# Performance work log

Measured on AMD Instinct MI355X. Metric: run time of the kernel, lower is better.

The kernel has to match this reference:

```python
import jax, jax.numpy as jnp
import numpy as np

EPS = 1e-5

def _subsys_level(x, W, b, g, beta):
    # x: [S,B,I], W: [S,O,I]  -> Linear -> Tanh -> BatchNorm(batch stats over B)
    h = jnp.einsum('sbi,soi->sbo', x, W) + b[:, None, :]
    h = jnp.tanh(h)
    mu = jnp.mean(h, axis=1, keepdims=True)
    var = jnp.var(h, axis=1, keepdims=True)
    return g[:, None, :] * (h - mu) * jax.lax.rsqrt(var + EPS) + beta[:, None, :]

def setup_inputs() -> dict:
    key = jax.random.key(0)
    ks = jax.random.split(key, 16)
    B, N = 4096, 6000
    u = lambda k, shp: jax.random.uniform(k, shp, jnp.float32, -0.001, 0.001)
    return {
        'mutant_state': jax.random.uniform(ks[0], (B, N), jnp.float32),
        'gene_idx': jax.random.randint(ks[1], (512, 16), 0, N),
        'W1': u(ks[2], (512, 20, 16)), 'b1': u(ks[3], (512, 20)),
        'g1': jnp.ones((512, 20), jnp.float32), 'beta1': jnp.zeros((512, 20), jnp.float32),
        'W2': u(ks[4], (64, 24, 160)), 'b2': u(ks[5], (64, 24)),
        'g2': jnp.ones((64, 24), jnp.float32), 'beta2': jnp.zeros((64, 24), jnp.float32),
        'W3': u(ks[6], (8, 32, 192)), 'b3': u(ks[7], (8, 32)),
        'g3': jnp.ones((8, 32), jnp.float32), 'beta3': jnp.zeros((8, 32), jnp.float32),
        'Wr': u(ks[8], (64, 256)), 'br': u(ks[9], (64,)),
        'gr': jnp.ones((64,), jnp.float32), 'betar': jnp.zeros((64,), jnp.float32),
    }

def reference(mutant_state, gene_idx, W1, b1, g1, beta1, W2, b2, g2, beta2,
              W3, b3, g3, beta3, Wr, br, gr, betar):
    B = mutant_state.shape[0]
    # Level 1 (leaves): gather per-term gene mutant states -> [S1,B,G]
    x1 = jnp.transpose(mutant_state[:, gene_idx], (1, 0, 2))  # [512,B,16]
    o1 = _subsys_level(x1, W1, b1, g1, beta1)                  # [512,B,20]
    # Level 2: each of 64 parents concatenates 8 children outputs -> [64,B,160]
    x2 = o1.reshape(64, 8, B, 20).transpose(0, 2, 1, 3).reshape(64, B, 160)
    o2 = _subsys_level(x2, W2, b2, g2, beta2)                  # [64,B,24]
    # Level 3: 8 parents x 8 children -> [8,B,192]
    x3 = o2.reshape(8, 8, B, 24).transpose(0, 2, 1, 3).reshape(8, B, 192)
    o3 = _subsys_level(x3, W3, b3, g3, beta3)                  # [8,B,32]
    # Root: concat 8 outputs -> [B,256]
    xr = o3.transpose(1, 0, 2).reshape(B, 256)
    hr = jnp.tanh(xr @ Wr.T + br)
    mu = jnp.mean(hr, axis=0, keepdims=True)
    var = jnp.var(hr, axis=0, keepdims=True)
    return gr * (hr - mu) * jax.lax.rsqrt(var + EPS) + betar  # [B,64]
```

## Files before the change

kernel.cpp:

```cpp
#include <hip/hip_runtime.h>
#include <hip/hip_fp16.h>

#define BATCH 4096
#define EPS 1e-5f

typedef __half h16;
typedef float f32x2 __attribute__((ext_vector_type(2)));

union H8 { float4 f4; h16 h[8]; };
union H4 { float2 f2; h16 h[4]; __half2 h2[2]; };
union H2U { float f; __half2 h2; unsigned int u; };

__device__ __forceinline__ float tanh_fast(float x){
  float e = __expf(2.0f*x);
  return 1.0f - 2.0f*__builtin_amdgcn_rcpf(e + 1.0f);
}

__device__ __forceinline__ float wred(float v){
  #pragma unroll
  for (int off=32; off; off>>=1) v += __shfl_xor(v, off);
  return v;
}

__global__ __launch_bounds__(256) void k_transpose(const float* __restrict__ ms, h16* __restrict__ msT){
  __shared__ float tile[64][65];
  int tc = blockIdx.x * 64;
  int tb = blockIdx.y * 64;
  int tx = threadIdx.x & 63;
  int ty = threadIdx.x >> 6;
  #pragma unroll
  for (int k=0;k<16;++k){
    int r = ty + k*4;
    int c = tc + tx;
    if (c < 6000) tile[r][tx] = ms[(size_t)(tb + r)*6000 + c];
  }
  __syncthreads();
  #pragma unroll
  for (int k=0;k<16;++k){
    int r = ty + k*4;
    int c = tc + r;
    if (c < 6000) msT[(size_t)c*BATCH + tb + tx] = __float2half(tile[tx][r]);
  }
}

__global__ __launch_bounds__(64) void k_statsA(const h16* __restrict__ msT, const int* __restrict__ gidx,
    const float* __restrict__ W1, const float* __restrict__ b1,
    h16* __restrict__ H1, float* __restrict__ part1){
  const int s = blockIdx.y;
  const int bc = blockIdx.x;
  const int lane = threadIdx.x;
  const int b0 = bc*256 + lane*4;
  const float* Wp = W1 + s*320;
  f32x2 acc[20][2];
  #pragma unroll
  for (int o=0;o<20;++o){
    float bv = b1[s*20+o];
    acc[o][0] = (f32x2){bv,bv};
    acc[o][1] = (f32x2){bv,bv};
  }
  #pragma unroll 4
  for (int g=0; g<16; ++g){
    const int row = gidx[s*16+g]*BATCH;
    H4 u; u.f2 = *reinterpret_cast<const float2*>(msT + row + b0);
    float2 fa = __half22float2(u.h2[0]);
    float2 fb = __half22float2(u.h2[1]);
    f32x2 xa = (f32x2){fa.x, fa.y};
    f32x2 xb = (f32x2){fb.x, fb.y};
    #pragma unroll
    for (int o=0;o<20;++o){
      float wv = Wp[o*16+g];
      f32x2 w2 = (f32x2){wv,wv};
      acc[o][0] = __builtin_elementwise_fma(xa, w2, acc[o][0]);
      acc[o][1] = __builtin_elementwise_fma(xb, w2, acc[o][1]);
    }
  }
  #pragma unroll
  for (int o=0;o<20;++o){
    float h0=tanh_fast(acc[o][0].x), h1=tanh_fast(acc[o][0].y);
    float h2=tanh_fast(acc[o][1].x), h3=tanh_fast(acc[o][1].y);
    H4 u;
    u.h2[0] = __float22half2_rn(make_float2(h0,h1));
    u.h2[1] = __float22half2_rn(make_float2(h2,h3));
    *reinterpret_cast<float2*>(H1 + (size_t)(s*20+o)*BATCH + b0) = u.f2;
    float S = wred((h0+h1)+(h2+h3));
    float Q = wred((h0*h0+h1*h1)+(h2*h2+h3*h3));
    if (lane==0){
      part1[((s*20+o)*2  )*16 + bc] = S;
      part1[((s*20+o)*2+1)*16 + bc] = Q;
    }
  }
}

__global__ __launch_bounds__(256) void k_fold2(const float* __restrict__ W, const float* __restrict__ bb,
    const float* __restrict__ g, const float* __restrict__ beta,
    const float* __restrict__ part, float* __restrict__ Wf, float* __restrict__ bf){
  const int p = blockIdx.x;
  const int tid = threadIdx.x;
  __shared__ float aL[160], cL[160];
  for (int t = tid; t < 160; t += 256){
    int ch = p*160 + t;
    float S=0.f, Q=0.f;
    for (int bc=0; bc<16; ++bc){ S += part[(ch*2)*16 + bc]; Q += part[(ch*2+1)*16 + bc]; }
    float mu  = S * (1.0f/BATCH);
    float var = Q * (1.0f/BATCH) - mu*mu;
    float a = g[ch] * rsqrtf(var + EPS);
    aL[t] = a;
    cL[t] = beta[ch] - a*mu;
  }
  __syncthreads();
  const int NW = 160*24;
  for (int e = tid; e < NW; e += 256){
    int j = e % 24, i = e / 24;
    Wf[p*NW + e] = W[p*NW + j*160 + i] * aL[i];
  }
  if (tid < 24){
    float sv = bb[p*24 + tid];
    for (int i=0;i<160;++i) sv = fmaf(W[p*NW + tid*160 + i], cL[i], sv);
    bf[p*24 + tid] = sv;
  }
}

__global__ __launch_bounds__(256) void k_passB(const h16* __restrict__ H1,
    const float* __restrict__ W2f, const float* __restrict__ b2f,
    h16* __restrict__ H2, float* __restrict__ part2){
  const int p = blockIdx.y;
  const int bc = blockIdx.x;
  const int tid = threadIdx.x;
  const int wv = tid >> 6;
  const int lane = tid & 63;
  const int b = bc*256 + wv*64 + lane;
  const int bcw = bc*4 + wv;
  f32x2 acc2[12];
  #pragma unroll
  for (int j2=0;j2<12;++j2) acc2[j2] = (f32x2){b2f[p*24+2*j2], b2f[p*24+2*j2+1]};
  const h16* __restrict__ h1p = H1 + (size_t)p*160*BATCH + b;
  const float* __restrict__ w2p = W2f + p*3840;
  #pragma unroll 4
  for (int i=0;i<160;++i){
    float x = __half2float(h1p[(size_t)i*BATCH]);
    f32x2 x2 = (f32x2){x,x};
    #pragma unroll
    for (int j2=0;j2<12;++j2){
      f32x2 w2 = (f32x2){w2p[i*24+2*j2], w2p[i*24+2*j2+1]};
      acc2[j2] = __builtin_elementwise_fma(x2, w2, acc2[j2]);
    }
  }
  float v[24];
  #pragma unroll
  for (int j2=0;j2<12;++j2){
    v[2*j2]   = tanh_fast(acc2[j2].x);
    v[2*j2+1] = tanh_fast(acc2[j2].y);
  }
  {
    h16* dst = H2 + ((size_t)p*BATCH + b)*24;
    H8 u;
    #pragma unroll
    for (int t=0;t<3;++t){
      #pragma unroll
      for (int j=0;j<8;++j) u.h[j] = __float2half(v[t*8+j]);
      *reinterpret_cast<float4*>(dst + t*8) = u.f4;
    }
  }
  #pragma unroll
  for (int j=0;j<24;++j){
    float S = wred(v[j]);
    float Q = wred(v[j]*v[j]);
    if (lane==0){
      part2[((p*24+j)*2  )*64 + bcw] = S;
      part2[((p*24+j)*2+1)*64 + bcw] = Q;
    }
  }
}

__global__ __launch_bounds__(512) void k_passC(const h16* __restrict__ H2, const float* __restrict__ part2,
    const float* __restrict__ g2, const float* __restrict__ beta2,
    const float* __restrict__ W3, const float* __restrict__ b3,
    h16* __restrict__ H3, float* __restrict__ part3){
  const int q = blockIdx.y;
  const int bc = blockIdx.x;
  const int tid = threadIdx.x;
  const int wv = tid >> 6;
  const int lane = tid & 63;
  __shared__ float aL[192], cL[192];
  for (int t = tid; t < 192; t += 512){
    int ch = q*192 + t;
    float S=0.f, Q=0.f;
    for (int c=0;c<64;++c){ S += part2[(ch*2)*64 + c]; Q += part2[(ch*2+1)*64 + c]; }
    float mu  = S * (1.0f/BATCH);
    float var = Q * (1.0f/BATCH) - mu*mu;
    float a = g2[ch] * rsqrtf(var + EPS);
    aL[t] = a; cL[t] = beta2[ch] - a*mu;
  }
  __syncthreads();
  const int b = bc*64 + lane;
  const int jb = wv*4;
  float acc[4];
  #pragma unroll
  for (int j=0;j<4;++j) acc[j] = b3[q*32 + jb + j];
  for (int c2=0;c2<8;++c2){
    const h16* src = H2 + ((size_t)(q*8+c2)*BATCH + b)*24;
    float xn[24];
    #pragma unroll
    for (int t=0;t<3;++t){
      H8 u; u.f4 = *reinterpret_cast<const float4*>(src + t*8);
      #pragma unroll
      for (int i=0;i<8;++i){
        int ci = c2*24 + t*8 + i;
        xn[t*8+i] = fmaf(aL[ci], __half2float(u.h[i]), cL[ci]);
      }
    }
    #pragma unroll
    for (int j=0;j<4;++j){
      const float* wr = W3 + q*6144 + (jb+j)*192 + c2*24;
      #pragma unroll
      for (int i=0;i<24;++i) acc[j] = fmaf(xn[i], wr[i], acc[j]);
    }
  }
  #pragma unroll
  for (int j=0;j<4;++j) acc[j] = tanh_fast(acc[j]);
  {
    h16* dst = H3 + (size_t)b*256 + q*32 + jb;
    H2U u0,u1;
    u0.h2 = __halves2half2(__float2half(acc[0]), __float2half(acc[1]));
    u1.h2 = __halves2half2(__float2half(acc[2]), __float2half(acc[3]));
    float2 vv; vv.x = u0.f; vv.y = u1.f;
    *reinterpret_cast<float2*>(dst) = vv;
  }
  #pragma unroll
  for (int j=0;j<4;++j){
    float S = wred(acc[j]);
    float Q = wred(acc[j]*acc[j]);
    if (lane==0){
      part3[((q*32+jb+j)*2  )*64 + bc] = S;
      part3[((q*32+jb+j)*2+1)*64 + bc] = Q;
    }
  }
}

__global__ __launch_bounds__(256) void k_passD(const h16* __restrict__ H3, const float* __restrict__ part3,
    const float* __restrict__ g3, const float* __restrict__ beta3,
    const float* __restrict__ Wr, const float* __restrict__ br,
    float* __restrict__ Hr, float* __restrict__ partR){
  const int bc = blockIdx.x;
  const int jb = blockIdx.y * 8;
  const int tid = threadIdx.x;
  const int wv = tid >> 6;
  const int lane = tid & 63;
  __shared__ float aL[256], cL[256];
  __shared__ float lacc[4][64][9];
  {
    float S=0.f, Q=0.f;
    for (int c=0;c<64;++c){ S += part3[(tid*2)*64 + c]; Q += part3[(tid*2+1)*64 + c]; }
    float mu  = S * (1.0f/BATCH);
    float var = Q * (1.0f/BATCH) - mu*mu;
    float a = g3[tid] * rsqrtf(var + EPS);
    aL[tid] = a; cL[tid] = beta3[tid] - a*mu;
  }
  __syncthreads();
  const int b = bc*64 + lane;
  float acc[8];
  #pragma unroll
  for (int j=0;j<8;++j) acc[j] = 0.f;
  const h16* src = H3 + (size_t)b*256 + wv*64;
  #pragma unroll
  for (int kk=0; kk<8; ++kk){
    const int sl = wv*8 + kk;
    H8 u; u.f4 = *reinterpret_cast<const float4*>(src + kk*8);
    float xn[8];
    #pragma unroll
    for (int i=0;i<8;++i){
      int ci = sl*8+i;
      xn[i] = fmaf(aL[ci], __half2float(u.h[i]), cL[ci]);
    }
    #pragma unroll
    for (int j=0;j<8;++j){
      const float* wr = Wr + (jb+j)*256 + sl*8;
      #pragma unroll
      for (int i=0;i<8;++i) acc[j] = fmaf(xn[i], wr[i], acc[j]);
    }
  }
  #pragma unroll
  for (int j=0;j<8;++j) lacc[wv][lane][j] = acc[j];
  __syncthreads();
  #pragma unroll
  for (int k=0;k<2;++k){
    const int j = k*4 + wv;
    float v = br[jb+j] + (lacc[0][lane][j] + lacc[1][lane][j]) + (lacc[2][lane][j] + lacc[3][lane][j]);
    v = tanh_fast(v);
    Hr[(size_t)b*64 + jb + j] = v;
    float S = wred(v);
    float Q = wred(v*v);
    if (lane==0){
      partR[((jb+j)*2  )*64 + bc] = S;
      partR[((jb+j)*2+1)*64 + bc] = Q;
    }
  }
}

__global__ __launch_bounds__(256) void k_final(const float* __restrict__ Hr, const float* __restrict__ partR,
    const float* __restrict__ gr, const float* __restrict__ betar, float* __restrict__ out){
  __shared__ float aL[64], cL[64];
  const int tid = threadIdx.x;
  if (tid < 64){
    float S=0.f, Q=0.f;
    for (int bc=0; bc<64; ++bc){ S += partR[(tid*2)*64 + bc]; Q += partR[(tid*2+1)*64 + bc]; }
    float mu  = S * (1.0f/BATCH);
    float var = Q * (1.0f/BATCH) - mu*mu;
    float a = gr[tid] * rsqrtf(var + EPS);
    aL[tid] = a; cL[tid] = betar[tid] - a*mu;
  }
  __syncthreads();
  const int i4 = blockIdx.x*256 + tid;
  float4 v = *reinterpret_cast<const float4*>(Hr + (size_t)i4*4);
  int o = (i4*4)&63;
  float4 r;
  r.x = aL[o  ]*v.x + cL[o  ];
  r.y = aL[o+1]*v.y + cL[o+1];
  r.z = aL[o+2]*v.z + cL[o+2];
  r.w = aL[o+3]*v.w + cL[o+3];
  *reinterpret_cast<float4*>(out + (size_t)i4*4) = r;
}

extern "C" void kernel_launch(void* const* d_in, const int* in_sizes, int n_in,
                              void* d_out, int out_size, void* d_ws, size_t ws_size,
                              hipStream_t stream) {
  const float* ms    = (const float*)d_in[0];
  const int*   gidx  = (const int*)  d_in[1];
  const float* W1    = (const float*)d_in[2];
  const float* b1    = (const float*)d_in[3];
  const float* g1    = (const float*)d_in[4];
  const float* beta1 = (const float*)d_in[5];
  const float* W2    = (const float*)d_in[6];
  const float* b2    = (const float*)d_in[7];
  const float* g2    = (const float*)d_in[8];
  const float* beta2 = (const float*)d_in[9];
  const float* W3    = (const float*)d_in[10];
  const float* b3    = (const float*)d_in[11];
  const float* g3    = (const float*)d_in[12];
  const float* beta3 = (const float*)d_in[13];
  const float* Wr    = (const float*)d_in[14];
  const float* br    = (const float*)d_in[15];
  const float* gr    = (const float*)d_in[16];
  const float* betar = (const float*)d_in[17];
  float* out = (float*)d_out;

  char* w = (char*)d_ws;
  size_t off = 0;
  auto take = [&](size_t bytes)->char*{
    char* p = w + off;
    off = (off + bytes + 255) & ~(size_t)255;
    return p;
  };
  h16*   msT    = (h16*)  take((size_t)6000*BATCH*2);
  h16*   H1     = (h16*)  take((size_t)10240*BATCH*2);
  h16*   H2     = (h16*)  take((size_t)64*BATCH*24*2);
  h16*   H3     = (h16*)  take((size_t)BATCH*256*2);
  float* Hr     = (float*)take((size_t)BATCH*64*4);
  float* part1  = (float*)take((size_t)10240*2*16*4);
  float* part2  = (float*)take((size_t)1536*2*64*4);
  float* part3  = (float*)take((size_t)256*2*64*4);
  float* partR  = (float*)take((size_t)64*2*64*4);
  float* W2f    = (float*)take((size_t)64*24*160*4);
  float* b2f    = (float*)take((size_t)64*24*4);
  if (off > ws_size) return;

  k_transpose<<<dim3(94,64), 256, 0, stream>>>(ms, msT);
  k_statsA<<<dim3(16,512), 64, 0, stream>>>(msT, gidx, W1, b1, H1, part1);
  k_fold2<<<64, 256, 0, stream>>>(W2, b2, g1, beta1, part1, W2f, b2f);
  k_passB<<<dim3(16,64), 256, 0, stream>>>(H1, W2f, b2f, H2, part2);
  k_passC<<<dim3(64,8), 512, 0, stream>>>(H2, part2, g2, beta2, W3, b3, H3, part3);
  k_passD<<<dim3(64,8), 256, 0, stream>>>(H3, part3, g3, beta3, Wr, br, Hr, partR);
  k_final<<<256, 256, 0, stream>>>(Hr, partR, gr, betar, out);
}
```

Measured before the change: 185.4 us.

## Store level-1 activations interleaved per batch pair and widen statsA blocks

k_statsA now processes two batch elements per thread with 256-thread blocks and writes its outputs in a layout where each batch pair's 20 channels sit contiguously as packed half2 words. Channel-major stride-BATCH rows are replaced with per-subsystem, per-batch-pair records. k_passB reads this new layout, and the partial-stat buffers double to 32 wave slots, with k_fold2 updated to sum them. The aim is higher occupancy in statsA and more contiguous stores, at the cost of strided 2-byte reads in passB that stride 40 halves per batch pair.

```diff
diff --git a/kernel.cpp b/kernel.cpp
--- a/kernel.cpp
+++ b/kernel.cpp
@@ -8,7 +8,6 @@
 typedef float f32x2 __attribute__((ext_vector_type(2)));
 
 union H8 { float4 f4; h16 h[8]; };
-union H4 { float2 f2; h16 h[4]; __half2 h2[2]; };
 union H2U { float f; __half2 h2; unsigned int u; };
 
 __device__ __forceinline__ float tanh_fast(float x){
@@ -43,50 +42,48 @@
   }
 }
 
-__global__ __launch_bounds__(64) void k_statsA(const h16* __restrict__ msT, const int* __restrict__ gidx,
+__global__ __launch_bounds__(256) void k_statsA(const h16* __restrict__ msT, const int* __restrict__ gidx,
     const float* __restrict__ W1, const float* __restrict__ b1,
-    h16* __restrict__ H1, float* __restrict__ part1){
+    float* __restrict__ H1f, float* __restrict__ part1){
   const int s = blockIdx.y;
   const int bc = blockIdx.x;
-  const int lane = threadIdx.x;
-  const int b0 = bc*256 + lane*4;
+  const int tid = threadIdx.x;
+  const int wv = tid >> 6;
+  const int lane = tid & 63;
+  const int bp = bc*256 + tid;
+  const int b0 = bp*2;
   const float* Wp = W1 + s*320;
-  f32x2 acc[20][2];
+  f32x2 acc[20];
   #pragma unroll
   for (int o=0;o<20;++o){
     float bv = b1[s*20+o];
-    acc[o][0] = (f32x2){bv,bv};
-    acc[o][1] = (f32x2){bv,bv};
+    acc[o] = (f32x2){bv,bv};
   }
   #pragma unroll 4
   for (int g=0; g<16; ++g){
     const int row = gidx[s*16+g]*BATCH;
-    H4 u; u.f2 = *reinterpret_cast<const float2*>(msT + row + b0);
-    float2 fa = __half22float2(u.h2[0]);
-    float2 fb = __half22float2(u.h2[1]);
-    f32x2 xa = (f32x2){fa.x, fa.y};
-    f32x2 xb = (f32x2){fb.x, fb.y};
+    H2U u; u.f = *reinterpret_cast<const float*>(msT + row + b0);
+    float2 f = __half22float2(u.h2);
+    f32x2 x2 = (f32x2){f.x, f.y};
     #pragma unroll
     for (int o=0;o<20;++o){
-      float wv = Wp[o*16+g];
-      f32x2 w2 = (f32x2){wv,wv};
-      acc[o][0] = __builtin_elementwise_fma(xa, w2, acc[o][0]);
-      acc[o][1] = __builtin_elementwise_fma(xb, w2, acc[o][1]);
-    }
-  }
+      float wv_ = Wp[o*16+g];
+      acc[o] = __builtin_elementwise_fma(x2, (f32x2){wv_,wv_}, acc[o]);
+    }
+  }
+  float* dst = H1f + ((size_t)s*2048 + bp)*20;
   #pragma unroll
   for (int o=0;o<20;++o){
-    float h0=tanh_fast(acc[o][0].x), h1=tanh_fast(acc[o][0].y);
-    float h2=tanh_fast(acc[o][1].x), h3=tanh_fast(acc[o][1].y);
-    H4 u;
-    u.h2[0] = __float22half2_rn(make_float2(h0,h1));
-    u.h2[1] = __float22half2_rn(make_float2(h2,h3));
-    *reinterpret_cast<float2*>(H1 + (size_t)(s*20+o)*BATCH + b0) = u.f2;
-    float S = wred((h0+h1)+(h2+h3));
-    float Q = wred((h0*h0+h1*h1)+(h2*h2+h3*h3));
+    float h0 = tanh_fast(acc[o].x);
+    float h1 = tanh_fast(acc[o].y);
+    H2U u; u.h2 = __float22half2_rn(make_float2(h0,h1));
+    dst[o] = u.f;
+    float S = wred(h0+h1);
+    float Q = wred(h0*h0+h1*h1);
     if (lane==0){
-      part1[((s*20+o)*2  )*16 + bc] = S;
-      part1[((s*20+o)*2+1)*16 + bc] = Q;
+      const int bcw = bc*4 + wv;
+      part1[((s*20+o)*2  )*32 + bcw] = S;
+      part1[((s*20+o)*2+1)*32 + bcw] = Q;
     }
   }
 }
@@ -100,7 +97,7 @@
   for (int t = tid; t < 160; t += 256){
     int ch = p*160 + t;
     float S=0.f, Q=0.f;
-    for (int bc=0; bc<16; ++bc){ S += part[(ch*2)*16 + bc]; Q += part[(ch*2+1)*16 + bc]; }
+    for (int bc=0; bc<32; ++bc){ S += part[(ch*2)*32 + bc]; Q += part[(ch*2+1)*32 + bc]; }
     float mu  = S * (1.0f/BATCH);
     float var = Q * (1.0f/BATCH) - mu*mu;
     float a = g[ch] * rsqrtf(var + EPS);
@@ -128,21 +125,26 @@
   const int tid = threadIdx.x;
   const int wv = tid >> 6;
   const int lane = tid & 63;
-  const int b = bc*256 + wv*64 + lane;
+  const int b = bc*256 + tid;
   const int bcw = bc*4 + wv;
   f32x2 acc2[12];
   #pragma unroll
   for (int j2=0;j2<12;++j2) acc2[j2] = (f32x2){b2f[p*24+2*j2], b2f[p*24+2*j2+1]};
-  const h16* __restrict__ h1p = H1 + (size_t)p*160*BATCH + b;
   const float* __restrict__ w2p = W2f + p*3840;
-  #pragma unroll 4
-  for (int i=0;i<160;++i){
-    float x = __half2float(h1p[(size_t)i*BATCH]);
-    f32x2 x2 = (f32x2){x,x};
-    #pragma unroll
-    for (int j2=0;j2<12;++j2){
-      f32x2 w2 = (f32x2){w2p[i*24+2*j2], w2p[i*24+2*j2+1]};
-      acc2[j2] = __builtin_elementwise_fma(x2, w2, acc2[j2]);
+  #pragma unroll
+  for (int c=0;c<8;++c){
+    const int s = p*8 + c;
+    const h16* __restrict__ hb = H1 + ((size_t)(s*2048 + (b>>1))*20)*2 + (b&1);
+    #pragma unroll 4
+    for (int o=0;o<20;++o){
+      float x = __half2float(hb[o*2]);
+      f32x2 x2 = (f32x2){x,x};
+      const float* wj = w2p + (c*20+o)*24;
+      #pragma unroll
+      for (int j2=0;j2<12;++j2){
+        f32x2 w2 = (f32x2){wj[2*j2], wj[2*j2+1]};
+        acc2[j2] = __builtin_elementwise_fma(x2, w2, acc2[j2]);
+      }
     }
   }
   float v[24];
@@ -352,11 +354,11 @@
     return p;
   };
   h16*   msT    = (h16*)  take((size_t)6000*BATCH*2);
-  h16*   H1     = (h16*)  take((size_t)10240*BATCH*2);
+  float* H1f    = (float*)take((size_t)512*2048*20*4);
   h16*   H2     = (h16*)  take((size_t)64*BATCH*24*2);
   h16*   H3     = (h16*)  take((size_t)BATCH*256*2);
   float* Hr     = (float*)take((size_t)BATCH*64*4);
-  float* part1  = (float*)take((size_t)10240*2*16*4);
+  float* part1  = (float*)take((size_t)10240*2*32*4);
   float* part2  = (float*)take((size_t)1536*2*64*4);
   float* part3  = (float*)take((size_t)256*2*64*4);
   float* partR  = (float*)take((size_t)64*2*64*4);
@@ -365,9 +367,9 @@
   if (off > ws_size) return;
 
   k_transpose<<<dim3(94,64), 256, 0, stream>>>(ms, msT);
-  k_statsA<<<dim3(16,512), 64, 0, stream>>>(msT, gidx, W1, b1, H1, part1);
+  k_statsA<<<dim3(8,512), 256, 0, stream>>>(msT, gidx, W1, b1, H1f, part1);
   k_fold2<<<64, 256, 0, stream>>>(W2, b2, g1, beta1, part1, W2f, b2f);
-  k_passB<<<dim3(16,64), 256, 0, stream>>>(H1, W2f, b2f, H2, part2);
+  k_passB<<<dim3(16,64), 256, 0, stream>>>((const h16*)H1f, W2f, b2f, H2, part2);
   k_passC<<<dim3(64,8), 512, 0, stream>>>(H2, part2, g2, beta2, W3, b3, H3, part3);
   k_passD<<<dim3(64,8), 256, 0, stream>>>(H3, part3, g3, beta3, Wr, br, Hr, partR);
   k_final<<<256, 256, 0, stream>>>(Hr, partR, gr, betar, out);
```

After: 252.0 us. 35.9% more time.
